# Optimization experiments

Hardware: AMD Instinct MI355X
Metric: run time of the kernel (lower is better)

## Reference

```python
import jax, jax.numpy as jnp
import numpy as np
from jax import lax

B, M, L = 4, 20, 200
IN_C, C1, C2 = 2048, 512, 256
CDIM, DC1, DC2, SDIM = 300, 512, 256, 1024
NEG = -1e15  # -INFINITY in source


def conv1d(x, w, b, pad):
    # x: [N, Cin, L], w: [Cout, Cin, K]
    y = lax.conv_general_dilated(x, w, (1,), ((pad, pad),),
                                 dimension_numbers=('NCH', 'OIH', 'NCH'))
    return y + b[None, :, None]


def maxpool2(x):
    return lax.reduce_window(x, -jnp.inf, lax.max, (1, 1, 2), (1, 1, 2), 'VALID')


def deconv1d(x, w, b):
    # torch ConvTranspose1d(k=4, s=2, p=1): conv with lhs_dilation=2, pad k-1-p=2,
    # kernel flipped and in/out swapped. w: [Cin, Cout, K]
    wt = jnp.flip(w, -1).transpose(1, 0, 2)  # [Cout, Cin, K]
    y = lax.conv_general_dilated(x, wt, (1,), ((2, 2),), lhs_dilation=(2,),
                                 dimension_numbers=('NCH', 'OIH', 'NCH'))
    return y + b[None, :, None]


def setup_inputs() -> dict:
    key = jax.random.key(0)
    ks = jax.random.split(key, 16)
    p = lambda k, sh, s=0.02: (jax.random.normal(k, sh, jnp.float32) * s)
    return dict(
        batch=jax.random.normal(ks[0], (B, M, L, IN_C), jnp.float32),
        seg_len=jax.random.randint(ks[1], (B, M), 1, L + 1, jnp.int32),
        concept1=jax.random.normal(ks[2], (B, CDIM), jnp.float32),
        concept2=jax.random.normal(ks[3], (B, CDIM), jnp.float32),
        w_conv1=p(ks[4], (C1, IN_C, 5)), b_conv1=jnp.zeros((C1,), jnp.float32),
        w_conv2=p(ks[5], (C2, C1, 5)), b_conv2=jnp.zeros((C2,), jnp.float32),
        w_ca1=p(ks[6], (C2, CDIM)), w_ca2=p(ks[7], (C2, C2)), w_ca3=p(ks[8], (1, C2)),
        w_dc1=p(ks[9], (3 * C2, DC1, 4)), b_dc1=jnp.zeros((DC1,), jnp.float32),
        w_dc2=p(ks[10], (DC1, DC2, 4)), b_dc2=jnp.zeros((DC2,), jnp.float32),
        w_sim1=p(ks[11], (SDIM, DC2)), w_sim2=p(ks[12], (SDIM, CDIM)),
        w_mlp=p(ks[13], (1, SDIM)), b_mlp=jnp.zeros((1,), jnp.float32),
    )


def reference(batch, seg_len, concept1, concept2,
              w_conv1, b_conv1, w_conv2, b_conv2,
              w_ca1, w_ca2, w_ca3,
              w_dc1, b_dc1, w_dc2, b_dc2,
              w_sim1, w_sim2, w_mlp, b_mlp):
    Bs, Ms, Ls = batch.shape[:3]
    Lq = Ls // 4
    x = batch.reshape(Bs * Ms, Ls, -1).transpose(0, 2, 1)        # [BM, IN_C, L]
    t1 = maxpool2(conv1d(x, w_conv1, b_conv1, 2))                # [BM, C1, L/2]
    t2 = maxpool2(conv1d(t1, w_conv2, b_conv2, 2)).transpose(0, 2, 1)  # [BM, L/4, C2]

    # vectorized ragged mask: k < ceil(seg_len/4)
    mask = (jnp.arange(Lq)[None, None, :] < ((seg_len + 3) // 4)[:, :, None])
    mask = mask.reshape(Bs * Ms, Lq)

    kproj = t2 @ w_ca2.T                                         # [BM, Lq, C2]

    def concept_att(concept):
        # additive attention; scores are identical across the query-frame dim,
        # so compute one row and broadcast the weighted sum.
        q = concept @ w_ca1.T                                    # [B, C2]
        qe = jnp.repeat(q, Ms, axis=0)                           # [BM, C2]
        s = jnp.tanh(qe[:, None, :] + kproj) @ w_ca3[0]          # [BM, Lq]
        s = jnp.where(mask, s, NEG)
        a = jax.nn.softmax(s, axis=-1)
        r = jnp.einsum('bk,bkc->bc', a, t2)                      # [BM, C2]
        return jnp.broadcast_to(r[:, None, :], t2.shape)         # [BM, Lq, C2]

    r1 = concept_att(concept1)
    r2 = concept_att(concept2)

    cat = jnp.concatenate([t2, r1, r2], axis=-1).transpose(0, 2, 1)  # [BM, 3C2, Lq]
    d = deconv1d(cat, w_dc1, b_dc1)                              # [BM, DC1, L/2]
    d = deconv1d(d, w_dc2, b_dc2).transpose(0, 2, 1)             # [BM, L, DC2]
    d = d.reshape(Bs, Ms * Ls, -1)

    sim1 = d @ w_sim1.T                                          # [B, M*L, SDIM]
    c1 = concept1 @ w_sim2.T                                     # [B, SDIM]
    c2 = concept2 @ w_sim2.T
    sc1 = jax.nn.sigmoid((c1[:, None, :] * sim1) @ w_mlp[0] + b_mlp[0])
    sc2 = jax.nn.sigmoid((c2[:, None, :] * sim1) @ w_mlp[0] + b_mlp[0])
    return sc1.reshape(Bs, Ms, Ls), sc2.reshape(Bs, Ms, Ls)
```

## Files before the change

kernel.cpp:

```cpp
#include <hip/hip_runtime.h>
#include <hip/hip_bf16.h>
#include <math.h>

#define BB 4
#define MM 20
#define LL 200
#define INC 2048
#define C1 512
#define C2 256
#define CDIM 300
#define DC1 512
#define DC2 256
#define SDIM 1024
#define BM 80
#define L2 100
#define L4 50

typedef unsigned short u16;
typedef __attribute__((ext_vector_type(8))) short bf16x8;
typedef __attribute__((ext_vector_type(4))) float f32x4;

__device__ __forceinline__ u16 f2bf_rne(float f) {
  unsigned u = __float_as_uint(f);
  unsigned r = u + 0x7FFFu + ((u >> 16) & 1u);
  return (u16)(r >> 16);
}
__device__ __forceinline__ float bf2f(u16 v) {
  return __uint_as_float(((unsigned)v) << 16);
}

__device__ __forceinline__ void gload16(const u16* g, u16* l) {
  __builtin_amdgcn_global_load_lds(
      (const __attribute__((address_space(1))) void*)g,
      (__attribute__((address_space(3))) void*)l, 16, 0, 0);
}

__global__ void k_cast_pad_batch(const float* __restrict__ in, u16* __restrict__ out) {
  int idx = blockIdx.x * 256 + threadIdx.x;
  if (idx >= 80 * 204 * 256) return;
  int c8 = idx % 256;
  int pi = (idx / 256) % 204;
  int n  = idx / (256 * 204);
  uint4 o = make_uint4(0u, 0u, 0u, 0u);
  if (pi >= 2 && pi < 202) {
    const float* p = in + ((long long)(n * 200 + pi - 2) * 2048 + c8 * 8);
    float4 a = *(const float4*)p;
    float4 b = *(const float4*)(p + 4);
    o.x = (unsigned)f2bf_rne(a.x) | ((unsigned)f2bf_rne(a.y) << 16);
    o.y = (unsigned)f2bf_rne(a.z) | ((unsigned)f2bf_rne(a.w) << 16);
    o.z = (unsigned)f2bf_rne(b.x) | ((unsigned)f2bf_rne(b.y) << 16);
    o.w = (unsigned)f2bf_rne(b.z) | ((unsigned)f2bf_rne(b.w) << 16);
  }
  int key = (n * 204 + pi) & 7;
  long long pos = ((long long)(n * 204 + pi)) * 256 + (c8 ^ key);
  *(uint4*)(out + pos * 8) = o;
}

__global__ void k_zero_pad(u16* __restrict__ p, int ncnt, int rpad, int lr, int P,
                           int cin8, int total) {
  int idx = blockIdx.x * 256 + threadIdx.x;
  if (idx >= total) return;
  int c = idx % cin8;
  int pr = (idx / cin8) % (rpad - lr);
  int n = idx / (cin8 * (rpad - lr));
  int row = (pr < P) ? pr : lr + pr;
  *(uint4*)(p + ((long long)(n * rpad + row) * cin8 + c) * 8) = make_uint4(0, 0, 0, 0);
}

__global__ void k_cast_bf16(const float* __restrict__ in, u16* __restrict__ out, int n8) {
  int idx = blockIdx.x * 256 + threadIdx.x;
  if (idx >= n8) return;
  const float4* p = (const float4*)in + (long long)idx * 2;
  float4 a = p[0], b = p[1];
  uint4 o;
  o.x = (unsigned)f2bf_rne(a.x) | ((unsigned)f2bf_rne(a.y) << 16);
  o.y = (unsigned)f2bf_rne(a.z) | ((unsigned)f2bf_rne(a.w) << 16);
  o.z = (unsigned)f2bf_rne(b.x) | ((unsigned)f2bf_rne(b.y) << 16);
  o.w = (unsigned)f2bf_rne(b.z) | ((unsigned)f2bf_rne(b.w) << 16);
  *(uint4*)(out + (long long)idx * 8) = o;
}

__global__ void k_conv_w_t(const float* __restrict__ in, u16* __restrict__ out,
                           int Cout, int Cin, int Kk) {
  int idx = blockIdx.x * 256 + threadIdx.x;
  int total = Cout * Cin * Kk;
  if (idx >= total) return;
  int ci = idx % Cin;
  int t  = (idx / Cin) % Kk;
  int co = idx / (Cin * Kk);
  out[idx] = f2bf_rne(in[(co * Cin + ci) * Kk + t]);
}

__global__ void k_deconv_w_par(const float* __restrict__ in, u16* __restrict__ out,
                               int Cin, int Cout) {
  int idx = blockIdx.x * 256 + threadIdx.x;
  int total = Cin * Cout * 4;
  if (idx >= total) return;
  int ci = idx % Cin;
  int tt = (idx / Cin) & 1;
  int co = (idx / (2 * Cin)) % Cout;
  int zz = idx / (2 * Cin * Cout);
  out[idx] = f2bf_rne(in[(ci * Cout + co) * 4 + 3 - zz - 2 * tt]);
}

__global__ __launch_bounds__(256) void k_prep_small(
    const float* __restrict__ concept1, const float* __restrict__ concept2,
    const float* __restrict__ w_ca1, const float* __restrict__ w_sim1,
    const float* __restrict__ w_sim2, const float* __restrict__ w_mlp,
    float* __restrict__ qv) {
  int cz = blockIdx.x >> 2;
  int b  = blockIdx.x & 3;
  const float* con = cz ? concept2 : concept1;
  __shared__ float cvec[CDIM];
  __shared__ float chat[SDIM];
  int tid = threadIdx.x;
  for (int j = tid; j < CDIM; j += 256) cvec[j] = con[b * CDIM + j];
  __syncthreads();
  float accq = 0.f;
  for (int j = 0; j < CDIM; ++j) accq += cvec[j] * w_ca1[tid * CDIM + j];
  qv[(cz * 4 + b) * 256 + tid] = accq;
  for (int i = 0; i < 4; ++i) {
    int s = tid + i * 256;
    float a2 = 0.f;
    for (int j = 0; j < CDIM; ++j) a2 += cvec[j] * w_sim2[s * CDIM + j];
    chat[s] = a2 * w_mlp[s];
  }
  __syncthreads();
  float v = 0.f;
  for (int s = 0; s < SDIM; ++s) v += w_sim1[s * 256 + tid] * chat[s];
  qv[2048 + (cz * 4 + b) * 256 + tid] = v;
}

template <int SWZO>
__global__ __launch_bounds__(256) void k_gemm_conv(
    const u16* __restrict__ A, const u16* __restrict__ Bw,
    u16* __restrict__ Co, const float* __restrict__ bias,
    int M, int N, int Ktot, int cin, int ncib,
    int lr, int rpad, int px, int yspan, int gy,
    int orpad, int ooff, long long aend) {
  __shared__ __align__(16) u16 At[2][10240];
  __shared__ __align__(16) u16 Bs[2][8192];
  int id = blockIdx.x;
  int k8 = id & 7, j = id >> 3;
  int x = k8 / px, h = k8 - x * px;
  int y = h * yspan + j;
  if (y >= gy) return;
  int row0 = y * 128, col0 = x * 128;
  int tid = threadIdx.x, w = tid >> 6, ln = tid & 63;
  int r15 = ln & 15, q = ln >> 4;

  int n0 = row0 / lr, l0 = row0 - n0 * lr;
  long long prow0 = (long long)n0 * rpad + l0;

  int wrb = (w >> 1) * 64;
  int rlb[4], pp[4];
  #pragma unroll
  for (int mi = 0; mi < 4; ++mi) {
    int rr = wrb + mi * 16 + r15;
    int nc = (row0 + rr) / lr - n0;
    rlb[mi] = rr + 4 * nc;
    pp[mi] = (int)((prow0 + rlb[mi]) & 7);
  }

  long long arow_base = prow0 + w * 40 + (ln >> 3);
  const u16* alim = A + (aend - 8);
  auto stA = [&](int cib_, int pc) {
    const u16* src = A + (arow_base + pc * 8) * cin + cib_ * 64 + (ln & 7) * 8;
    if (src > alim) src = alim;
    gload16(src, At[cib_ & 1] + (w * 40 + pc * 8) * 64);
  };

  const u16* gb[4];
  #pragma unroll
  for (int i = 0; i < 4; ++i) {
    int f = 4 * w + i, blk = f >> 1, ks = f & 1;
    int klocal = ks * 32 + q * 8;
    int br = col0 + blk * 16 + r15;
    gb[i] = Bw + ((long long)br * Ktot + klocal);
  }
  int wbase = 4 * w * 512;

  f32x4 acc[4][4];
  #pragma unroll
  for (int i = 0; i < 4; ++i)
    #pragma unroll
    for (int j2 = 0; j2 < 4; ++j2) acc[i][j2] = (f32x4){0.f, 0.f, 0.f, 0.f};
  int wc2 = (w & 1) * 4;

  #pragma unroll
  for (int pc = 0; pc < 5; ++pc) stA(0, pc);
  #pragma unroll
  for (int i = 0; i < 4; ++i) gload16(gb[i], Bs[0] + wbase + i * 512);
  #pragma unroll
  for (int i = 0; i < 4; ++i) gb[i] += cin;
  int ts = 1;
  asm volatile("s_waitcnt vmcnt(0)" ::: "memory");
  __builtin_amdgcn_s_barrier();

  long long bwrap = 64 - 4 * (long long)cin;
  for (int cib = 0; cib < ncib; ++cib) {
    bool lastcib = (cib == ncib - 1);
    #pragma unroll
    for (int t = 0; t < 5; ++t) {
      bool lastc = lastcib && (t == 4);
      if (!lastcib) stA(cib + 1, t);
      if (!lastc) {
        int bufn = (cib + t + 1) & 1;
        #pragma unroll
        for (int i = 0; i < 4; ++i) gload16(gb[i], Bs[bufn] + wbase + i * 512);
        long long d = (ts == 4) ? bwrap : (long long)cin;
        ts = (ts == 4) ? 0 : ts + 1;
        #pragma unroll
        for (int i = 0; i < 4; ++i) gb[i] += d;
      }
      if (lastc)        asm volatile("s_waitcnt vmcnt(0)" ::: "memory");
      else if (lastcib) asm volatile("s_waitcnt vmcnt(4)" ::: "memory");
      else              asm volatile("s_waitcnt vmcnt(5)" ::: "memory");
      __builtin_amdgcn_s_barrier();
      __builtin_amdgcn_sched_barrier(0);
      const u16* Ab = At[cib & 1];
      const u16* Bb = Bs[(cib + t) & 1];
      int rof[4], pr8[4];
      #pragma unroll
      for (int mi = 0; mi < 4; ++mi) {
        rof[mi] = (rlb[mi] + t) * 64;
        pr8[mi] = (pp[mi] + t) & 7;
      }
      #pragma unroll
      for (int ks = 0; ks < 2; ++ks) {
        bf16x8 af[4], bf[4];
        #pragma unroll
        for (int mi = 0; mi < 4; ++mi)
          af[mi] = *(const bf16x8*)&Ab[rof[mi] + (((ks * 4 + q) ^ pr8[mi]) * 8)];
        #pragma unroll
        for (int ni = 0; ni < 4; ++ni)
          bf[ni] = *(const bf16x8*)&Bb[(((wc2 + ni) * 2 + ks) * 512) + ln * 8];
        #pragma unroll
        for (int mi = 0; mi < 4; ++mi)
          #pragma unroll
          for (int ni = 0; ni < 4; ++ni)
            acc[mi][ni] = __builtin_amdgcn_mfma_f32_16x16x32_bf16(
                af[mi], bf[ni], acc[mi][ni], 0, 0, 0);
      }
      __builtin_amdgcn_sched_barrier(0);
      __builtin_amdgcn_s_barrier();
    }
  }

  int q4 = q * 4;
  int wrow = (w >> 1) * 64, wcol = (w & 1) * 64;
  int lrh = lr >> 1;
  #pragma unroll
  for (int mi = 0; mi < 4; ++mi) {
    int gbase = row0 + wrow + mi * 16 + q4;
    #pragma unroll
    for (int p = 0; p < 2; ++p) {
      int grow = gbase + 2 * p;
      if (grow < M) {
        int prow = grow >> 1;
        int n = prow / lrh, ll = prow - n * lrh;
        long long orow = (long long)n * orpad + ooff + ll;
        int key = SWZO ? ((int)(orow & 7) << 3) : 0;
        #pragma unroll
        for (int ni = 0; ni < 4; ++ni) {
          int col = col0 + wcol + ni * 16 + r15;
          float v = fmaxf(acc[mi][ni][2 * p], acc[mi][ni][2 * p + 1]) + bias[col];
          Co[orow * N + (col ^ key)] = f2bf_rne(v);
        }
      }
    }
  }
}

#define EP_PLAIN 0
#define EP_POOL  1
#define EP_ILV   2

template <int EP>
__global__ __launch_bounds__(256) void k_gemm(
    const u16* __restrict__ A, const u16* __restrict__ Bw,
    void* __restrict__ Co, const float* __restrict__ bias,
    int M, int N, int Ktot, int nchunk,
    int lr, int rpad, int cin, int off0c, int taps,
    int px, int yspan, int gy, long long sB, int orpad, int ooff) {
  __shared__ __align__(16) u16 As[2][8192];
  __shared__ __align__(16) u16 Bs[2][8192];
  int id = blockIdx.x;
  int k8 = id & 7, j = id >> 3;
  int x = k8 / px, h = k8 - x * px;
  int y = h * yspan + j;
  if (y >= gy) return;
  int z = blockIdx.z;
  int off0 = (EP == EP_ILV) ? z : off0c;
  int row0 = y * 128, col0 = x * 128;
  int tid = threadIdx.x, w = tid >> 6, ln = tid & 63;
  const u16* Bz = Bw + (long long)z * sB;

  const u16* ga[4];
  const u16* gb[4];
  #pragma unroll
  for (int i = 0; i < 4; ++i) {
    int f = 4 * w + i, blk = f >> 1, ks = f & 1;
    int klocal = ks * 32 + (ln >> 4) * 8;
    int ar = row0 + blk * 16 + (ln & 15);
    int n_ = ar / lr, l_ = ar - n_ * lr;
    ga[i] = A + ((long long)(n_ * rpad + l_ + off0) * cin + klocal);
    int br = col0 + blk * 16 + (ln & 15);
    gb[i] = Bz + ((long long)br * Ktot + klocal);
  }
  int wbase = 4 * w * 512;

  f32x4 acc[4][4];
  #pragma unroll
  for (int i = 0; i < 4; ++i)
    #pragma unroll
    for (int j2 = 0; j2 < 4; ++j2) acc[i][j2] = (f32x4){0.f, 0.f, 0.f, 0.f};

  int wr2 = (w >> 1) * 4;
  int wc2 = (w & 1) * 4;

  long long dstep = cin;
  long long dwrap = 64 - (long long)(taps - 1) * cin;
  int tc = 0;

  #pragma unroll
  for (int i = 0; i < 4; ++i) {
    gload16(ga[i], As[0] + wbase + i * 512);
    gload16(gb[i], Bs[0] + wbase + i * 512);
  }
  {
    long long d = (tc == taps - 1) ? dwrap : dstep;
    tc = (tc == taps - 1) ? 0 : tc + 1;
    #pragma unroll
    for (int i = 0; i < 4; ++i) { ga[i] += d; gb[i] += d; }
  }

  for (int c = 0; c < nchunk; ++c) {
    int cur = c & 1;
    if (c + 1 < nchunk) {
      u16* dA = As[cur ^ 1] + wbase;
      u16* dB = Bs[cur ^ 1] + wbase;
      #pragma unroll
      for (int i = 0; i < 4; ++i) {
        gload16(ga[i], dA + i * 512);
        gload16(gb[i], dB + i * 512);
      }
      long long d = (tc == taps - 1) ? dwrap : dstep;
      tc = (tc == taps - 1) ? 0 : tc + 1;
      #pragma unroll
      for (int i = 0; i < 4; ++i) { ga[i] += d; gb[i] += d; }
      asm volatile("s_waitcnt vmcnt(8)" ::: "memory");
    } else {
      asm volatile("s_waitcnt vmcnt(0)" ::: "memory");
    }
    __builtin_amdgcn_s_barrier();
    __builtin_amdgcn_sched_barrier(0);
    #pragma unroll
    for (int ks = 0; ks < 2; ++ks) {
      bf16x8 af[4], bf[4];
      #pragma unroll
      for (int mi = 0; mi < 4; ++mi)
        af[mi] = *(const bf16x8*)&As[cur][(((wr2 + mi) * 2 + ks) * 512) + ln * 8];
      #pragma unroll
      for (int ni = 0; ni < 4; ++ni)
        bf[ni] = *(const bf16x8*)&Bs[cur][(((wc2 + ni) * 2 + ks) * 512) + ln * 8];
      #pragma unroll
      for (int mi = 0; mi < 4; ++mi)
        #pragma unroll
        for (int ni = 0; ni < 4; ++ni)
          acc[mi][ni] = __builtin_amdgcn_mfma_f32_16x16x32_bf16(
              af[mi], bf[ni], acc[mi][ni], 0, 0, 0);
    }
    __builtin_amdgcn_sched_barrier(0);
    __builtin_amdgcn_s_barrier();
  }

  int c15 = ln & 15, q4 = (ln >> 4) * 4;
  int wrow = (w >> 1) * 64, wcol = (w & 1) * 64;
  if (EP == EP_PLAIN) {
    float* Cz = (float*)Co;
    #pragma unroll
    for (int mi = 0; mi < 4; ++mi) {
      int gbase = row0 + wrow + mi * 16 + q4;
      #pragma unroll
      for (int r = 0; r < 4; ++r) {
        int grow = gbase + r;
        if (grow < M) {
          #pragma unroll
          for (int ni = 0; ni < 4; ++ni) {
            int col = col0 + wcol + ni * 16 + c15;
            Cz[(long long)grow * N + col] = acc[mi][ni][r];
          }
        }
      }
    }
  } else if (EP == EP_POOL) {
    u16* Cz = (u16*)Co;
    int lrh = lr >> 1;
    #pragma unroll
    for (int mi = 0; mi < 4; ++mi) {
      int gbase = row0 + wrow + mi * 16 + q4;
      #pragma unroll
      for (int p = 0; p < 2; ++p) {
        int grow = gbase + 2 * p;
        if (grow < M) {
          int prow = grow >> 1;
          int n = prow / lrh, ll = prow - n * lrh;
          long long orow = (long long)n * orpad + ooff + ll;
          #pragma unroll
          for (int ni = 0; ni < 4; ++ni) {
            int col = col0 + wcol + ni * 16 + c15;
            float v = fmaxf(acc[mi][ni][2 * p], acc[mi][ni][2 * p + 1]) + bias[col];
            Cz[orow * N + col] = f2bf_rne(v);
          }
        }
      }
    }
  } else {
    u16* Cz = (u16*)Co;
    #pragma unroll
    for (int mi = 0; mi < 4; ++mi) {
      int gbase = row0 + wrow + mi * 16 + q4;
      #pragma unroll
      for (int r = 0; r < 4; ++r) {
        int grow = gbase + r;
        if (grow < M) {
          int n = grow / lr, l = grow - n * lr;
          long long orow = (long long)n * orpad + ooff + 2 * l + z;
          #pragma unroll
          for (int ni = 0; ni < 4; ++ni) {
            int col = col0 + wcol + ni * 16 + c15;
            Cz[orow * N + col] = f2bf_rne(acc[mi][ni][r] + bias[col]);
          }
        }
      }
    }
  }
}

__global__ __launch_bounds__(256) void k_attention(
    const float* __restrict__ kproj, const u16* __restrict__ t2b,
    const float* __restrict__ qv, const float* __restrict__ w_ca3,
    const int* __restrict__ seg_len, u16* __restrict__ rb) {
  int bm = blockIdx.x % BM;
  int cz = blockIdx.x / BM;
  int b = bm / MM;
  int tid = threadIdx.x, w = tid >> 6, ln = tid & 63;
  __shared__ float sq[256], sw[256], sa[L4 + 14];
  sq[tid] = qv[(cz * 4 + b) * 256 + tid];
  sw[tid] = w_ca3[tid];
  __syncthreads();
  int kmax = (seg_len[bm] + 3) >> 2;
  for (int k = w; k < L4; k += 4) {
    float val = 0.f;
    #pragma unroll
    for (int i = 0; i < 4; ++i) {
      int c = ln + 64 * i;
      val += tanhf(sq[c] + kproj[(bm * L4 + k) * 256 + c]) * sw[c];
    }
    for (int off = 32; off > 0; off >>= 1) val += __shfl_down(val, off, 64);
    if (ln == 0) sa[k] = (k < kmax) ? val : -1e15f;
  }
  __syncthreads();
  if (w == 0) {
    float sv = (ln < L4) ? sa[ln] : -3e38f;
    float mx = sv;
    for (int off = 32; off > 0; off >>= 1) mx = fmaxf(mx, __shfl_down(mx, off, 64));
    mx = __shfl(mx, 0, 64);
    float e = (ln < L4) ? expf(sv - mx) : 0.f;
    float s = e;
    for (int off = 32; off > 0; off >>= 1) s += __shfl_down(s, off, 64);
    s = __shfl(s, 0, 64);
    if (ln < L4) sa[ln] = e / s;
  }
  __syncthreads();
  float r = 0.f;
  for (int k = 0; k < L4; ++k) r += sa[k] * bf2f(t2b[(bm * L4 + k) * 256 + tid]);
  rb[(cz * BM + bm) * 256 + tid] = f2bf_rne(r);
}

__global__ void k_build_cat(const u16* __restrict__ t2b, const u16* __restrict__ rb,
                            u16* __restrict__ catm, int total) {
  int idx = blockIdx.x * 256 + threadIdx.x;
  if (idx >= total) return;
  int ci = idx % 768;
  int row = idx / 768;
  int bm = row / L4, li = row - bm * L4;
  u16 v;
  if (ci < 256)      v = t2b[row * 256 + ci];
  else if (ci < 512) v = rb[bm * 256 + (ci - 256)];
  else               v = rb[(BM + bm) * 256 + (ci - 512)];
  catm[((long long)(bm * 52 + 1 + li)) * 768 + ci] = v;
}

__global__ __launch_bounds__(256) void k_final(
    const u16* __restrict__ d2b, const float* __restrict__ qv,
    const float* __restrict__ b_mlp, float* __restrict__ out) {
  int row = blockIdx.x;
  int n = row / LL, lo = row % LL;
  int b = n / MM, m = n % MM;
  int tid = threadIdx.x;
  float v = bf2f(d2b[(long long)row * 256 + tid]);
  float p1 = v * qv[2048 + (0 * 4 + b) * 256 + tid];
  float p2 = v * qv[2048 + (1 * 4 + b) * 256 + tid];
  for (int off = 32; off > 0; off >>= 1) {
    p1 += __shfl_down(p1, off, 64);
    p2 += __shfl_down(p2, off, 64);
  }
  __shared__ float s1[4], s2[4];
  if ((tid & 63) == 0) { s1[tid >> 6] = p1; s2[tid >> 6] = p2; }
  __syncthreads();
  if (tid == 0) {
    float bmlp = b_mlp[0];
    float a1 = s1[0] + s1[1] + s1[2] + s1[3] + bmlp;
    float a2 = s2[0] + s2[1] + s2[2] + s2[3] + bmlp;
    int t_idx = m * LL + lo;
    out[b * 4000 + t_idx]         = 1.f / (1.f + expf(-a1));
    out[16000 + b * 4000 + t_idx] = 1.f / (1.f + expf(-a2));
  }
}

extern "C" void kernel_launch(void* const* d_in, const int* in_sizes, int n_in,
                              void* d_out, int out_size, void* d_ws, size_t ws_size,
                              hipStream_t stream) {
  const float* batch    = (const float*)d_in[0];
  const int*   seg_len  = (const int*)d_in[1];
  const float* concept1 = (const float*)d_in[2];
  const float* concept2 = (const float*)d_in[3];
  const float* w_conv1  = (const float*)d_in[4];
  const float* b_conv1  = (const float*)d_in[5];
  const float* w_conv2  = (const float*)d_in[6];
  const float* b_conv2  = (const float*)d_in[7];
  const float* w_ca1    = (const float*)d_in[8];
  const float* w_ca2    = (const float*)d_in[9];
  const float* w_ca3    = (const float*)d_in[10];
  const float* w_dc1    = (const float*)d_in[11];
  const float* b_dc1    = (const float*)d_in[12];
  const float* w_dc2    = (const float*)d_in[13];
  const float* b_dc2    = (const float*)d_in[14];
  const float* w_sim1   = (const float*)d_in[15];
  const float* w_sim2   = (const float*)d_in[16];
  const float* w_mlp    = (const float*)d_in[17];
  const float* b_mlp    = (const float*)d_in[18];
  float* out = (float*)d_out;

  float* ws = (float*)d_ws;
  const long long off_qv    = 0;
  const long long off_kproj = 4096;
  const long long off_rb    = 1028096;
  const long long off_t1    = 1048576;
  const long long off_t2    = 3211264;
  const long long off_w1b   = 3735552;
  const long long off_w2b   = 6356992;
  const long long off_wd1p  = 6684672;
  const long long off_wd2p  = 7471104;
  const long long off_wca2b = 7733248;
  const long long off_BIG   = 7766016;

  u16* rb    = (u16*)(ws + off_rb);
  u16* t1b   = (u16*)(ws + off_t1);
  u16* t2b   = (u16*)(ws + off_t2);
  u16* w1b   = (u16*)(ws + off_w1b);
  u16* w2b   = (u16*)(ws + off_w2b);
  u16* wd1p  = (u16*)(ws + off_wd1p);
  u16* wd2p  = (u16*)(ws + off_wd2p);
  u16* wca2b = (u16*)(ws + off_wca2b);
  u16* batchb = (u16*)(ws + off_BIG);
  u16* catm   = (u16*)(ws + off_BIG);
  u16* d1b    = (u16*)(ws + off_BIG) + 3342336;
  u16* d2b    = (u16*)(ws + off_BIG) + 7667712;

  k_cast_pad_batch<<<dim3(16320), 256, 0, stream>>>(batch, batchb);
  k_conv_w_t<<<dim3(20480), 256, 0, stream>>>(w_conv1, w1b, C1, INC, 5);
  k_conv_w_t<<<dim3(2560), 256, 0, stream>>>(w_conv2, w2b, C2, C1, 5);
  k_deconv_w_par<<<dim3(6144), 256, 0, stream>>>(w_dc1, wd1p, 3 * C2, DC1);
  k_deconv_w_par<<<dim3(2048), 256, 0, stream>>>(w_dc2, wd2p, DC1, DC2);
  k_cast_bf16<<<dim3(32), 256, 0, stream>>>(w_ca2, wca2b, 8192);
  k_prep_small<<<dim3(8), 256, 0, stream>>>(concept1, concept2, w_ca1, w_sim1, w_sim2,
                                            w_mlp, ws + off_qv);
  k_zero_pad<<<dim3(80), 256, 0, stream>>>(t1b, 80, 104, 100, 2, 64, 20480);

  k_gemm_conv<1><<<dim3(504), 256, 0, stream>>>(
      batchb, w1b, t1b, b_conv1, 16000, 512, 10240, 2048, 32,
      200, 204, 2, 63, 125, 104, 2, 80LL * 204 * 2048);

  k_zero_pad<<<dim3(60), 256, 0, stream>>>(catm, 80, 52, 50, 1, 96, 15360);
  k_zero_pad<<<dim3(40), 256, 0, stream>>>(d1b, 80, 102, 100, 1, 64, 10240);

  k_gemm_conv<0><<<dim3(128), 256, 0, stream>>>(
      t1b, w2b, t2b, b_conv2, 8000, 256, 2560, 512, 8,
      100, 104, 4, 16, 63, 50, 0, 80LL * 104 * 512);

  k_gemm<EP_PLAIN><<<dim3(64), 256, 0, stream>>>(
      t2b, wca2b, ws + off_kproj, nullptr, 4000, 256, 256, 4,
      4000, 4000, 256, 0, 1, 4, 8, 32, 0, 0, 0);

  k_attention<<<dim3(160), 256, 0, stream>>>(ws + off_kproj, t2b, ws + off_qv,
                                             w_ca3, seg_len, rb);

  k_build_cat<<<dim3(12000), 256, 0, stream>>>(t2b, rb, catm, 4000 * 768);

  k_gemm<EP_ILV><<<dim3(128, 1, 2), 256, 0, stream>>>(
      catm, wd1p, d1b, b_dc1, 4000, 512, 1536, 24,
      50, 52, 768, 0, 2, 2, 16, 32, 786432LL, 102, 1);

  k_gemm<EP_ILV><<<dim3(128, 1, 2), 256, 0, stream>>>(
      d1b, wd2p, d2b, b_dc2, 8000, 256, 1024, 16,
      100, 102, 512, 0, 2, 4, 16, 63, 262144LL, 200, 0);

  k_final<<<dim3(16000), 256, 0, stream>>>(d2b, ws + off_qv, b_mlp, out);
}
```

Before: 749.8 us.

## Use 256x128 tiles with 512-thread blocks for the first conv GEMM

Adds a dedicated conv1 implicit-GEMM kernel that computes 256-row by 128-column output tiles with 8 waves per block instead of 128x128 tiles with 4 waves. Each B-weight tile loaded into shared memory is now reused across twice as many rows, which cuts global weight traffic and halves the number of blocks (504 down to 256). In exchange the block needs more LDS (a larger A buffer) and can hit occupancy or tail-balance problems with fewer, larger blocks.

```diff
diff --git a/kernel.cpp b/kernel.cpp
--- a/kernel.cpp
+++ b/kernel.cpp
@@ -129,6 +129,144 @@
   float v = 0.f;
   for (int s = 0; s < SDIM; ++s) v += w_sim1[s * 256 + tid] * chat[s];
   qv[2048 + (cz * 4 + b) * 256 + tid] = v;
+}
+
+__global__ __launch_bounds__(512) void k_gemm_conv1(
+    const u16* __restrict__ A, const u16* __restrict__ Bw,
+    u16* __restrict__ Co, const float* __restrict__ bias,
+    int M, int N, int Ktot, int cin, int ncib,
+    int lr, int rpad, int px, int yspan, int gy,
+    int orpad, int ooff, long long aend) {
+  __shared__ __align__(16) u16 At[2][20480];
+  __shared__ __align__(16) u16 Bs[2][8192];
+  int id = blockIdx.x;
+  int k8 = id & 7, j = id >> 3;
+  int x = k8 / px, h = k8 - x * px;
+  int y = h * yspan + j;
+  if (y >= gy) return;
+  int row0 = y * 256, col0 = x * 128;
+  int tid = threadIdx.x, w = tid >> 6, ln = tid & 63;
+  int r15 = ln & 15, q = ln >> 4;
+
+  int n0 = row0 / lr, l0 = row0 - n0 * lr;
+  long long prow0 = (long long)n0 * rpad + l0;
+
+  int wrb = (w >> 1) * 64;
+  int rlb[4], pp[4];
+  #pragma unroll
+  for (int mi = 0; mi < 4; ++mi) {
+    int rr = wrb + mi * 16 + r15;
+    int nc = (row0 + rr) / lr - n0;
+    rlb[mi] = rr + 4 * nc;
+    pp[mi] = (int)((prow0 + rlb[mi]) & 7);
+  }
+
+  long long arow_base = prow0 + w * 40 + (ln >> 3);
+  const u16* alim = A + (aend - 8);
+  auto stA = [&](int cib_, int pc) {
+    const u16* src = A + (arow_base + pc * 8) * cin + cib_ * 64 + (ln & 7) * 8;
+    if (src > alim) src = alim;
+    gload16(src, At[cib_ & 1] + (w * 40 + pc * 8) * 64);
+  };
+
+  const u16* gb[2];
+  #pragma unroll
+  for (int i = 0; i < 2; ++i) {
+    int klocal = i * 32 + q * 8;
+    int br = col0 + w * 16 + r15;
+    gb[i] = Bw + ((long long)br * Ktot + klocal);
+  }
+
+  f32x4 acc[4][4];
+  #pragma unroll
+  for (int i = 0; i < 4; ++i)
+    #pragma unroll
+    for (int j2 = 0; j2 < 4; ++j2) acc[i][j2] = (f32x4){0.f, 0.f, 0.f, 0.f};
+  int wc2 = (w & 1) * 4;
+
+  #pragma unroll
+  for (int pc = 0; pc < 5; ++pc) stA(0, pc);
+  #pragma unroll
+  for (int i = 0; i < 2; ++i) gload16(gb[i], Bs[0] + (2 * w + i) * 512);
+  #pragma unroll
+  for (int i = 0; i < 2; ++i) gb[i] += cin;
+  int ts = 1;
+  asm volatile("s_waitcnt vmcnt(0)" ::: "memory");
+  __builtin_amdgcn_s_barrier();
+
+  long long bwrap = 64 - 4 * (long long)cin;
+  for (int cib = 0; cib < ncib; ++cib) {
+    bool lastcib = (cib == ncib - 1);
+    #pragma unroll
+    for (int t = 0; t < 5; ++t) {
+      bool lastc = lastcib && (t == 4);
+      if (!lastcib) stA(cib + 1, t);
+      if (!lastc) {
+        int bufn = (cib + t + 1) & 1;
+        #pragma unroll
+        for (int i = 0; i < 2; ++i) gload16(gb[i], Bs[bufn] + (2 * w + i) * 512);
+        long long d = (ts == 4) ? bwrap : (long long)cin;
+        ts = (ts == 4) ? 0 : ts + 1;
+        #pragma unroll
+        for (int i = 0; i < 2; ++i) gb[i] += d;
+      }
+      if (lastc)        asm volatile("s_waitcnt vmcnt(0)" ::: "memory");
+      else if (lastcib) asm volatile("s_waitcnt vmcnt(2)" ::: "memory");
+      else              asm volatile("s_waitcnt vmcnt(3)" ::: "memory");
+      __builtin_amdgcn_s_barrier();
+      __builtin_amdgcn_sched_barrier(0);
+      const u16* Ab = At[cib & 1];
+      const u16* Bb = Bs[(cib + t) & 1];
+      int rof[4], pr8[4];
+      #pragma unroll
+      for (int mi = 0; mi < 4; ++mi) {
+        rof[mi] = (rlb[mi] + t) * 64;
+        pr8[mi] = (pp[mi] + t) & 7;
+      }
+      #pragma unroll
+      for (int ks = 0; ks < 2; ++ks) {
+        bf16x8 af[4], bf[4];
+        #pragma unroll
+        for (int mi = 0; mi < 4; ++mi)
+          af[mi] = *(const bf16x8*)&Ab[rof[mi] + (((ks * 4 + q) ^ pr8[mi]) * 8)];
+        #pragma unroll
+        for (int ni = 0; ni < 4; ++ni)
+          bf[ni] = *(const bf16x8*)&Bb[(((wc2 + ni) * 2 + ks) * 512) + ln * 8];
+        #pragma unroll
+        for (int mi = 0; mi < 4; ++mi)
+          #pragma unroll
+          for (int ni = 0; ni < 4; ++ni)
+            acc[mi][ni] = __builtin_amdgcn_mfma_f32_16x16x32_bf16(
+                af[mi], bf[ni], acc[mi][ni], 0, 0, 0);
+      }
+      __builtin_amdgcn_sched_barrier(0);
+      __builtin_amdgcn_s_barrier();
+    }
+  }
+
+  int q4 = q * 4;
+  int wrow = (w >> 1) * 64, wcol = (w & 1) * 64;
+  int lrh = lr >> 1;
+  #pragma unroll
+  for (int mi = 0; mi < 4; ++mi) {
+    int gbase = row0 + wrow + mi * 16 + q4;
+    #pragma unroll
+    for (int p = 0; p < 2; ++p) {
+      int grow = gbase + 2 * p;
+      if (grow < M) {
+        int prow = grow >> 1;
+        int n = prow / lrh, ll = prow - n * lrh;
+        long long orow = (long long)n * orpad + ooff + ll;
+        int key = (int)(orow & 7) << 3;
+        #pragma unroll
+        for (int ni = 0; ni < 4; ++ni) {
+          int col = col0 + wcol + ni * 16 + r15;
+          float v = fmaxf(acc[mi][ni][2 * p], acc[mi][ni][2 * p + 1]) + bias[col];
+          Co[orow * N + (col ^ key)] = f2bf_rne(v);
+        }
+      }
+    }
+  }
 }
 
 template <int SWZO>
@@ -580,9 +718,9 @@
                                             w_mlp, ws + off_qv);
   k_zero_pad<<<dim3(80), 256, 0, stream>>>(t1b, 80, 104, 100, 2, 64, 20480);
 
-  k_gemm_conv<1><<<dim3(504), 256, 0, stream>>>(
+  k_gemm_conv1<<<dim3(256), 512, 0, stream>>>(
       batchb, w1b, t1b, b_conv1, 16000, 512, 10240, 2048, 32,
-      200, 204, 2, 63, 125, 104, 2, 80LL * 204 * 2048);
+      200, 204, 2, 32, 63, 104, 2, 80LL * 204 * 2048);
 
   k_zero_pad<<<dim3(60), 256, 0, stream>>>(catm, 80, 52, 50, 1, 96, 15360);
   k_zero_pad<<<dim3(40), 256, 0, stream>>>(d1b, 80, 102, 100, 1, 64, 10240);
```

Measured after the change: 768.7 us. 2.5% more time.
